# Performance work log

Hardware: AMD Instinct MI355X
Metric: run time of the kernel (lower is better)

## Reference

```python
import jax, jax.numpy as jnp
import numpy as np

NOISE_STD = 0.1
NUM_EXPERTS = 32
TOPK = 2
OUTPUT_DIM = 256


def setup_inputs() -> dict:
    key = jax.random.key(0)
    k_x, k_n, k_gw, k_ew = jax.random.split(key, 4)
    N, D_IN = 32768, 256
    E, D_OUT = NUM_EXPERTS, OUTPUT_DIM
    x = jax.random.normal(k_x, (N, D_IN), dtype=jnp.float32)
    noise = jax.random.normal(k_n, (N, E), dtype=jnp.float32)
    # gate: nn.Linear(input_dim, num_experts) default init scale
    gate_w = jax.random.normal(k_gw, (E, D_IN), dtype=jnp.float32) / jnp.sqrt(D_IN).astype(jnp.float32)
    gate_b = jnp.zeros((E,), dtype=jnp.float32)
    # experts: nn.Linear(input_dim, output_dim * num_experts), xavier_uniform weight, zero bias
    lim = float(np.sqrt(6.0 / (D_IN + D_OUT * E)))
    experts_w = jax.random.uniform(k_ew, (D_OUT * E, D_IN), minval=-lim, maxval=lim, dtype=jnp.float32)
    experts_b = jnp.zeros((D_OUT * E,), dtype=jnp.float32)
    return {"x": x, "noise": noise, "gate_w": gate_w, "gate_b": gate_b,
            "experts_w": experts_w, "experts_b": experts_b}


def reference(x, noise, gate_w, gate_b, experts_w, experts_b):
    N = x.shape[0]
    E, D = NUM_EXPERTS, OUTPUT_DIM
    # gating with noisy logits
    gate_logits = x @ gate_w.T + gate_b + noise * NOISE_STD          # [N, E]
    gate_probs = jax.nn.softmax(gate_logits, axis=-1)                # [N, E]
    # load-balance auxiliary loss
    gate_probs_mean = gate_probs.mean(axis=0)                        # [E]
    expected = 1.0 / E
    load_balance_loss = jnp.mean((gate_probs_mean - expected) ** 2) * E
    # top-k routing
    topk_probs, topk_idx = jax.lax.top_k(gate_probs, TOPK)           # [N, k]
    # all-expert dense linear, then gather the selected experts
    expert_outputs = (x @ experts_w.T + experts_b).reshape(N, E, D)  # [N, E, D]
    sel = jnp.take_along_axis(expert_outputs, topk_idx[:, :, None], axis=1)  # [N, k, D]
    output = jnp.einsum('bk,bkd->bd', topk_probs, sel)               # [N, D]
    return output, load_balance_loss
```

## Files before the change

kernel.cpp:

```cpp
#include <hip/hip_runtime.h>
#include <hip/hip_bf16.h>

#define N_ROWS 32768
#define D_INP  256
#define NEXP   32
#define D_OUTP 256
#define TROWS  64
#define NTILES 1056
#define GROWS  64

typedef __attribute__((ext_vector_type(4))) float f32x4;
typedef __attribute__((ext_vector_type(8))) short bf16x8;

__device__ inline unsigned short f2b(float f) {
    union { __hip_bfloat16 h; unsigned short u; } cv;
    cv.h = __float2bfloat16(f);
    return cv.u;
}
__device__ inline float b2f(unsigned short u) {
    union { unsigned v; float f; } c; c.v = ((unsigned)u) << 16; return c.f;
}

__global__ __launch_bounds__(256) void gate_kernel(
    const float* __restrict__ x, const float* __restrict__ noise,
    const float* __restrict__ gw, const float* __restrict__ gb,
    const float* __restrict__ ew, unsigned short* __restrict__ wbT,
    unsigned short* __restrict__ xb, float* __restrict__ tkp,
    int* __restrict__ tki, float* __restrict__ esum, int* __restrict__ ecnt)
{
    __shared__ float rA[8448];
    __shared__ float xs[64 * 68];
    __shared__ float lsum[NEXP];
    __shared__ int   lcnt[NEXP];

    int tid = threadIdx.x;
    int row0 = blockIdx.x * GROWS;

    #pragma unroll
    for (int it = 0; it < 8; ++it) {
        int q = it * 256 + tid;
        int e = q >> 6;
        int k = (q & 63) * 4;
        float4 v = ((const float4*)gw)[q];
        *(float4*)&rA[e * 260 + k] = v;
    }
    if (tid < NEXP) { lsum[tid] = 0.f; lcnt[tid] = 0; }

    int lane = tid & 63;
    int wid  = tid >> 6;
    int e4 = lane & 7;
    int rq = lane >> 3;

    float acc[8][4];
    #pragma unroll
    for (int m = 0; m < 8; m++)
        #pragma unroll
        for (int n = 0; n < 4; n++) acc[m][n] = 0.f;

    for (int s = 0; s < 4; ++s) {
        __syncthreads();
        #pragma unroll
        for (int it = 0; it < 4; ++it) {
            int q = it * 256 + tid;
            int r = q >> 4;
            int kq = q & 15;
            float4 v = *(const float4*)(x + (size_t)(row0 + r) * D_INP + s * 64 + kq * 4);
            *(float4*)&xs[r * 68 + kq * 4] = v;
            unsigned short b[4] = { f2b(v.x), f2b(v.y), f2b(v.z), f2b(v.w) };
            *(ushort4*)(xb + (size_t)(row0 + r) * D_INP + s * 64 + kq * 4) = *(ushort4*)b;
        }
        __syncthreads();
        int ko = s * 64 + wid * 16;
        #pragma unroll
        for (int c = 0; c < 4; ++c) {
            float4 wv[4];
            #pragma unroll
            for (int n = 0; n < 4; n++)
                wv[n] = *(float4*)&rA[(e4 + 8 * n) * 260 + ko + c * 4];
            #pragma unroll
            for (int m = 0; m < 8; m++) {
                float4 xv = *(float4*)&xs[(rq + 8 * m) * 68 + wid * 16 + c * 4];
                #pragma unroll
                for (int n = 0; n < 4; n++)
                    acc[m][n] = fmaf(xv.x, wv[n].x,
                                fmaf(xv.y, wv[n].y,
                                fmaf(xv.z, wv[n].z,
                                fmaf(xv.w, wv[n].w, acc[m][n]))));
            }
        }
    }
    __syncthreads();

    {
        int base = (wid * 64 + lane) * 33;
        #pragma unroll
        for (int m = 0; m < 8; m++)
            #pragma unroll
            for (int n = 0; n < 4; n++)
                rA[base + m * 4 + n] = acc[m][n];
    }
    __syncthreads();

    {
        int row = tid >> 2;
        int eo  = (tid & 3) * 8;
        int n   = tid & 3;
        int R = row0 + row;
        int j = (row >> 3) * 4 + n;
        int lpb = (row & 7) * 8;
        float4 nz0 = *(const float4*)(noise + (size_t)R * NEXP + eo);
        float4 nz1 = *(const float4*)(noise + (size_t)R * NEXP + eo + 4);
        float nz[8] = { nz0.x, nz0.y, nz0.z, nz0.w, nz1.x, nz1.y, nz1.z, nz1.w };
        float l[8], p[8];
        #pragma unroll
        for (int i = 0; i < 8; i++) {
            int a = (lpb + i) * 33 + j;
            float v = rA[a] + rA[2112 + a] + rA[4224 + a] + rA[6336 + a];
            l[i] = v + gb[eo + i] + 0.1f * nz[i];
        }
        float mx = l[0];
        #pragma unroll
        for (int i = 1; i < 8; i++) mx = fmaxf(mx, l[i]);
        mx = fmaxf(mx, __shfl_xor(mx, 1));
        mx = fmaxf(mx, __shfl_xor(mx, 2));
        float sum = 0.f;
        #pragma unroll
        for (int i = 0; i < 8; i++) { p[i] = expf(l[i] - mx); sum += p[i]; }
        sum += __shfl_xor(sum, 1);
        sum += __shfl_xor(sum, 2);
        float inv = 1.f / sum;
        #pragma unroll
        for (int i = 0; i < 8; i++) p[i] *= inv;

        float bp = p[0]; int bi = eo;
        #pragma unroll
        for (int i = 1; i < 8; i++) if (p[i] > bp) { bp = p[i]; bi = eo + i; }
        #pragma unroll
        for (int s2 = 1; s2 < 4; s2 <<= 1) {
            float op = __shfl_xor(bp, s2); int oi = __shfl_xor(bi, s2);
            if (op > bp || (op == bp && oi < bi)) { bp = op; bi = oi; }
        }
        float bp2 = -1.f; int bi2 = 0;
        #pragma unroll
        for (int i = 0; i < 8; i++) {
            int E = eo + i;
            float q = (E == bi) ? -1.f : p[i];
            if (q > bp2 || (q == bp2 && E < bi2)) { bp2 = q; bi2 = E; }
        }
        #pragma unroll
        for (int s2 = 1; s2 < 4; s2 <<= 1) {
            float op = __shfl_xor(bp2, s2); int oi = __shfl_xor(bi2, s2);
            if (op > bp2 || (op == bp2 && oi < bi2)) { bp2 = op; bi2 = oi; }
        }
        if ((tid & 3) == 0) {
            tkp[R * 2] = bp;  tkp[R * 2 + 1] = bp2;
            tki[R * 2] = bi;  tki[R * 2 + 1] = bi2;
            atomicAdd(&lcnt[bi], 1); atomicAdd(&lcnt[bi2], 1);
        }
        #pragma unroll
        for (int i = 0; i < 8; i++) atomicAdd(&lsum[eo + i], p[i]);
    }

    #pragma unroll
    for (int it = 0; it < 2; ++it) {
        int fid = blockIdx.x * 512 + it * 256 + tid;
        int row = fid >> 5;
        int kc  = fid & 31;
        const float4* sp = (const float4*)(ew + (size_t)row * D_INP + kc * 8);
        float4 v0 = sp[0], v1 = sp[1];
        unsigned short t[8] = { f2b(v0.x), f2b(v0.y), f2b(v0.z), f2b(v0.w),
                                f2b(v1.x), f2b(v1.y), f2b(v1.z), f2b(v1.w) };
        int e  = row >> 8;
        int rr = row & 255;
        int q  = rr >> 6;
        int nn = (rr >> 4) & 3;
        int lr = rr & 15;
        int kk = kc >> 2;
        int kg = kc & 3;
        size_t off = ((((size_t)(e * 4 + q) * 8 + kk) * 4 + nn) * 64 + kg * 16 + lr) * 8;
        *(uint4*)(wbT + off) = *(uint4*)t;
    }

    __syncthreads();
    if (tid < NEXP) {
        unsafeAtomicAdd(&esum[tid], lsum[tid]);
        atomicAdd(&ecnt[tid], lcnt[tid]);
    }
}

__global__ __launch_bounds__(1024) void build_list_kernel(
    const int* __restrict__ tki, const float* __restrict__ esum,
    const int* __restrict__ ecnt, int* __restrict__ cursor0,
    int* __restrict__ list, float* __restrict__ loss_out)
{
    __shared__ int lcnt[NEXP], lbase[NEXP], s_offs[NEXP + 1];
    int tid = threadIdx.x;
    if (tid < NEXP) lcnt[tid] = 0;
    if (tid < 32) {
        int c = ecnt[tid];
        int ic = c;
        #pragma unroll
        for (int s = 1; s < 32; s <<= 1) {
            int a = __shfl_up(ic, s, 32);
            if (tid >= s) ic += a;
        }
        s_offs[tid + 1] = ic;
        if (tid == 0) s_offs[0] = 0;
    }
    __syncthreads();
    int r = blockIdx.x * 1024 + tid;
    int e0 = tki[r * 2], e1 = tki[r * 2 + 1];
    int p0 = atomicAdd(&lcnt[e0], 1);
    int p1 = atomicAdd(&lcnt[e1], 1);
    __syncthreads();
    if (tid < NEXP) lbase[tid] = s_offs[tid] + atomicAdd(&cursor0[tid], lcnt[tid]);
    __syncthreads();
    list[lbase[e0] + p0] = r * 2;
    list[lbase[e1] + p1] = r * 2 + 1;

    if (blockIdx.x == 0 && tid < 32) {
        float d = esum[tid] * (1.f / N_ROWS) - (1.f / NEXP);
        float v = d * d;
        #pragma unroll
        for (int s = 16; s > 0; s >>= 1) v += __shfl_xor(v, s, 32);
        if (tid == 0) *loss_out = v;
    }
}

__global__ __launch_bounds__(256) void moe_gemm_kernel(
    const unsigned short* __restrict__ xb, const unsigned short* __restrict__ wbT,
    const float* __restrict__ expb, const float* __restrict__ tkp,
    const int* __restrict__ list, const int* __restrict__ ecnt,
    unsigned short* __restrict__ y0, unsigned short* __restrict__ y1)
{
    __shared__ int s_offs[NEXP + 1], s_toff[NEXP + 1];
    __shared__ unsigned short xa[TROWS * 256];
    __shared__ int   srow[TROWS];
    __shared__ int   sslot[TROWS];
    __shared__ float sprob[TROWS];

    int tid = threadIdx.x;
    if (tid < 32) {
        int c = ecnt[tid];
        int ic = c, itc = (c + TROWS - 1) >> 6;
        #pragma unroll
        for (int s = 1; s < 32; s <<= 1) {
            int a  = __shfl_up(ic, s, 32);  if (tid >= s) ic += a;
            int b2 = __shfl_up(itc, s, 32); if (tid >= s) itc += b2;
        }
        s_offs[tid + 1] = ic; s_toff[tid + 1] = itc;
        if (tid == 0) { s_offs[0] = 0; s_toff[0] = 0; }
    }
    __syncthreads();

    int b = (blockIdx.x & 7) * (NTILES / 8) + (blockIdx.x >> 3);
    if (b >= s_toff[NEXP]) return;
    int e = 0;
    #pragma unroll
    for (int s = 16; s; s >>= 1)
        if (e + s <= 31 && s_toff[e + s] <= b) e += s;
    int m0 = s_offs[e] + (b - s_toff[e]) * TROWS;
    int nr = min(TROWS, s_offs[e + 1] - m0);

    if (tid < TROWS) {
        if (tid < nr) {
            int ent = list[m0 + tid];
            srow[tid]  = ent >> 1;
            sslot[tid] = ent & 1;
            sprob[tid] = tkp[ent];
        } else { srow[tid] = -1; sslot[tid] = 0; sprob[tid] = 0.f; }
    }
    __syncthreads();

    {
        int r_ = tid >> 2;
        int gr = srow[r_]; if (gr < 0) gr = 0;
        const uint4* src = (const uint4*)(xb + (size_t)gr * D_INP);
        uint4* dst = (uint4*)xa;
        int swz = r_ & 7;
        #pragma unroll
        for (int i = 0; i < 8; ++i) {
            int c = (tid & 3) + 4 * i;
            dst[r_ * 32 + (c ^ swz)] = src[c];
        }
    }
    __syncthreads();

    int wave = tid >> 6;
    int lane = tid & 63;
    int lr = lane & 15;
    int kg = lane >> 4;
    int n0 = wave * 64;
    int aswz = lr & 7;

    const unsigned short* wbase = wbT + (size_t)(e * 4 + wave) * 32 * 512;

    f32x4 acc[4][4];
    #pragma unroll
    for (int mm = 0; mm < 4; mm++)
        #pragma unroll
        for (int nn = 0; nn < 4; nn++)
            acc[mm][nn] = (f32x4){0.f, 0.f, 0.f, 0.f};

    #pragma unroll
    for (int kk = 0; kk < 8; kk++) {
        int chunk = kk * 4 + kg;
        bf16x8 a[4], bb[4];
        #pragma unroll
        for (int mm = 0; mm < 4; mm++)
            a[mm] = *(const bf16x8*)&xa[(mm * 16 + lr) * 256 + ((chunk ^ aswz) * 8)];
        #pragma unroll
        for (int nn = 0; nn < 4; nn++)
            bb[nn] = *(const bf16x8*)(wbase + (kk * 4 + nn) * 512 + lane * 8);
        #pragma unroll
        for (int mm = 0; mm < 4; mm++)
            #pragma unroll
            for (int nn = 0; nn < 4; nn++)
                acc[mm][nn] = __builtin_amdgcn_mfma_f32_16x16x32_bf16(a[mm], bb[nn], acc[mm][nn], 0, 0, 0);
    }
    __syncthreads();

    {
        float bias[4];
        #pragma unroll
        for (int nn = 0; nn < 4; nn++) bias[nn] = expb[e * 256 + n0 + nn * 16 + lr];
        #pragma unroll
        for (int mm = 0; mm < 4; mm++) {
            #pragma unroll
            for (int j = 0; j < 4; j++) {
                int lrow = mm * 16 + kg * 4 + j;
                float pp = sprob[lrow];
                #pragma unroll
                for (int nn = 0; nn < 4; nn++) {
                    float v = (acc[mm][nn][j] + bias[nn]) * pp;
                    xa[lrow * 256 + n0 + nn * 16 + lr] = f2b(v);
                }
            }
        }
    }
    __syncthreads();

    {
        int r_ = tid >> 2;
        int gr = srow[r_];
        if (gr >= 0) {
            unsigned short* dstb = (sslot[r_] ? y1 : y0) + (size_t)gr * D_OUTP;
            const uint4* src = (const uint4*)(xa + r_ * 256);
            uint4* dst = (uint4*)dstb;
            #pragma unroll
            for (int i = 0; i < 8; ++i) {
                int c = (tid & 3) + 4 * i;
                dst[c] = src[c];
            }
        }
    }
}

__global__ __launch_bounds__(256) void combine_kernel(
    const unsigned short* __restrict__ y0, const unsigned short* __restrict__ y1,
    float* __restrict__ out)
{
    size_t i = ((size_t)blockIdx.x * 256 + threadIdx.x) * 8;
    uint4 a = *(const uint4*)(y0 + i);
    uint4 b = *(const uint4*)(y1 + i);
    const unsigned short* ap = (const unsigned short*)&a;
    const unsigned short* bp = (const unsigned short*)&b;
    float4 o0, o1;
    o0.x = b2f(ap[0]) + b2f(bp[0]);
    o0.y = b2f(ap[1]) + b2f(bp[1]);
    o0.z = b2f(ap[2]) + b2f(bp[2]);
    o0.w = b2f(ap[3]) + b2f(bp[3]);
    o1.x = b2f(ap[4]) + b2f(bp[4]);
    o1.y = b2f(ap[5]) + b2f(bp[5]);
    o1.z = b2f(ap[6]) + b2f(bp[6]);
    o1.w = b2f(ap[7]) + b2f(bp[7]);
    *(float4*)(out + i)     = o0;
    *(float4*)(out + i + 4) = o1;
}

extern "C" void kernel_launch(void* const* d_in, const int* in_sizes, int n_in,
                              void* d_out, int out_size, void* d_ws, size_t ws_size,
                              hipStream_t stream)
{
    const float* x   = (const float*)d_in[0];
    const float* noi = (const float*)d_in[1];
    const float* gw  = (const float*)d_in[2];
    const float* gb  = (const float*)d_in[3];
    const float* ew  = (const float*)d_in[4];
    const float* eb  = (const float*)d_in[5];
    float* out = (float*)d_out;

    char* p = (char*)d_ws;
    unsigned short* xb  = (unsigned short*)p; p += (size_t)N_ROWS * D_INP * 2;
    unsigned short* wbT = (unsigned short*)p; p += (size_t)NEXP * D_OUTP * D_INP * 2;
    unsigned short* y0  = (unsigned short*)p; p += (size_t)N_ROWS * D_OUTP * 2;
    unsigned short* y1  = (unsigned short*)p; p += (size_t)N_ROWS * D_OUTP * 2;
    float* tkp  = (float*)p; p += (size_t)N_ROWS * 2 * 4;
    int*   tki  = (int*)p;   p += (size_t)N_ROWS * 2 * 4;
    int*   list = (int*)p;   p += (size_t)N_ROWS * 2 * 4;
    float* esum = (float*)p; p += 32 * 4;
    int*   ecnt = (int*)p;   p += 32 * 4;
    int*   cur0 = (int*)p;   p += 32 * 4;

    hipMemsetAsync(esum, 0, 3 * 32 * 4, stream);

    gate_kernel<<<N_ROWS / GROWS, 256, 0, stream>>>(x, noi, gw, gb, ew, wbT, xb, tkp, tki, esum, ecnt);
    build_list_kernel<<<N_ROWS / 1024, 1024, 0, stream>>>(tki, esum, ecnt, cur0, list, out + (size_t)N_ROWS * D_OUTP);
    moe_gemm_kernel<<<NTILES, 256, 0, stream>>>(xb, wbT, eb, tkp, list, ecnt, y0, y1);
    combine_kernel<<<N_ROWS * D_OUTP / 8 / 256, 256, 0, stream>>>(y0, y1, out);
}
```

Before: 149.1 us.

## Make MoE GEMM persistent per expert with register-prefetched next tile

Replaces the flat grid of 1056 single-tile blocks with 512 blocks, 16 per expert, each looping over that expert's row tiles with a stride of 16. The gathered x rows for the next tile are loaded into registers while the current tile's MFMA runs, so the gather latency is meant to overlap with compute. Routing entries for two tiles are staged in shared memory at once. This depends on the 16 blocks per expert covering load imbalance. Experts with more tiles take proportionally longer, and the extra register buffer may reduce occupancy.

```diff
diff --git a/kernel.cpp b/kernel.cpp
--- a/kernel.cpp
+++ b/kernel.cpp
@@ -6,7 +6,7 @@
 #define NEXP   32
 #define D_OUTP 256
 #define TROWS  64
-#define NTILES 1056
+#define NBLK   512
 #define GROWS  64
 
 typedef __attribute__((ext_vector_type(4))) float f32x4;
@@ -233,125 +233,147 @@
     const int* __restrict__ list, const int* __restrict__ ecnt,
     unsigned short* __restrict__ y0, unsigned short* __restrict__ y1)
 {
-    __shared__ int s_offs[NEXP + 1], s_toff[NEXP + 1];
+    __shared__ int s_offs[NEXP + 1];
     __shared__ unsigned short xa[TROWS * 256];
-    __shared__ int   srow[TROWS];
-    __shared__ int   sslot[TROWS];
-    __shared__ float sprob[TROWS];
+    __shared__ int   entT[2][TROWS];
+    __shared__ float sprobT[2][TROWS];
 
     int tid = threadIdx.x;
     if (tid < 32) {
         int c = ecnt[tid];
-        int ic = c, itc = (c + TROWS - 1) >> 6;
+        int ic = c;
         #pragma unroll
         for (int s = 1; s < 32; s <<= 1) {
-            int a  = __shfl_up(ic, s, 32);  if (tid >= s) ic += a;
-            int b2 = __shfl_up(itc, s, 32); if (tid >= s) itc += b2;
-        }
-        s_offs[tid + 1] = ic; s_toff[tid + 1] = itc;
-        if (tid == 0) { s_offs[0] = 0; s_toff[0] = 0; }
-    }
-    __syncthreads();
-
-    int b = (blockIdx.x & 7) * (NTILES / 8) + (blockIdx.x >> 3);
-    if (b >= s_toff[NEXP]) return;
-    int e = 0;
-    #pragma unroll
-    for (int s = 16; s; s >>= 1)
-        if (e + s <= 31 && s_toff[e + s] <= b) e += s;
-    int m0 = s_offs[e] + (b - s_toff[e]) * TROWS;
-    int nr = min(TROWS, s_offs[e + 1] - m0);
-
-    if (tid < TROWS) {
-        if (tid < nr) {
-            int ent = list[m0 + tid];
-            srow[tid]  = ent >> 1;
-            sslot[tid] = ent & 1;
-            sprob[tid] = tkp[ent];
-        } else { srow[tid] = -1; sslot[tid] = 0; sprob[tid] = 0.f; }
-    }
-    __syncthreads();
-
-    {
-        int r_ = tid >> 2;
-        int gr = srow[r_]; if (gr < 0) gr = 0;
-        const uint4* src = (const uint4*)(xb + (size_t)gr * D_INP);
-        uint4* dst = (uint4*)xa;
-        int swz = r_ & 7;
-        #pragma unroll
-        for (int i = 0; i < 8; ++i) {
-            int c = (tid & 3) + 4 * i;
-            dst[r_ * 32 + (c ^ swz)] = src[c];
-        }
-    }
-    __syncthreads();
+            int a = __shfl_up(ic, s, 32);
+            if (tid >= s) ic += a;
+        }
+        s_offs[tid + 1] = ic;
+        if (tid == 0) s_offs[0] = 0;
+    }
+    __syncthreads();
+
+    int bs = (blockIdx.x & 7) * 64 + (blockIdx.x >> 3);
+    int e  = bs >> 4;
+    int j0 = bs & 15;
+    int base  = s_offs[e];
+    int cnt   = s_offs[e + 1] - base;
+    int ntile = (cnt + TROWS - 1) >> 6;
+    if (j0 >= ntile) return;
 
     int wave = tid >> 6;
     int lane = tid & 63;
     int lr = lane & 15;
     int kg = lane >> 4;
     int n0 = wave * 64;
+    int sr = tid >> 2;
+    int sc = tid & 3;
+    int swz = sr & 7;
     int aswz = lr & 7;
 
     const unsigned short* wbase = wbT + (size_t)(e * 4 + wave) * 32 * 512;
-
-    f32x4 acc[4][4];
+    float bias[4];
     #pragma unroll
-    for (int mm = 0; mm < 4; mm++)
-        #pragma unroll
-        for (int nn = 0; nn < 4; nn++)
-            acc[mm][nn] = (f32x4){0.f, 0.f, 0.f, 0.f};
-
-    #pragma unroll
-    for (int kk = 0; kk < 8; kk++) {
-        int chunk = kk * 4 + kg;
-        bf16x8 a[4], bb[4];
-        #pragma unroll
-        for (int mm = 0; mm < 4; mm++)
-            a[mm] = *(const bf16x8*)&xa[(mm * 16 + lr) * 256 + ((chunk ^ aswz) * 8)];
-        #pragma unroll
-        for (int nn = 0; nn < 4; nn++)
-            bb[nn] = *(const bf16x8*)(wbase + (kk * 4 + nn) * 512 + lane * 8);
-        #pragma unroll
-        for (int mm = 0; mm < 4; mm++)
-            #pragma unroll
-            for (int nn = 0; nn < 4; nn++)
-                acc[mm][nn] = __builtin_amdgcn_mfma_f32_16x16x32_bf16(a[mm], bb[nn], acc[mm][nn], 0, 0, 0);
-    }
-    __syncthreads();
-
-    {
-        float bias[4];
-        #pragma unroll
-        for (int nn = 0; nn < 4; nn++) bias[nn] = expb[e * 256 + n0 + nn * 16 + lr];
-        #pragma unroll
-        for (int mm = 0; mm < 4; mm++) {
-            #pragma unroll
-            for (int j = 0; j < 4; j++) {
-                int lrow = mm * 16 + kg * 4 + j;
-                float pp = sprob[lrow];
-                #pragma unroll
-                for (int nn = 0; nn < 4; nn++) {
-                    float v = (acc[mm][nn][j] + bias[nn]) * pp;
-                    xa[lrow * 256 + n0 + nn * 16 + lr] = f2b(v);
+    for (int nn = 0; nn < 4; nn++) bias[nn] = expb[e * 256 + n0 + nn * 16 + lr];
+
+    uint4 areg[8];
+
+    for (int t0 = j0; t0 < ntile; t0 += 32) {
+        if (tid < 128) {
+            int p = tid >> 6, r = tid & 63;
+            int tp = t0 + p * 16;
+            int ent = -1; float pr = 0.f;
+            if (tp < ntile && r < cnt - tp * TROWS) {
+                ent = list[base + tp * TROWS + r];
+                pr  = tkp[ent];
+            }
+            entT[p][r] = ent; sprobT[p][r] = pr;
+        }
+        __syncthreads();
+
+        {
+            int ent = entT[0][sr];
+            int gr = ent < 0 ? 0 : (ent >> 1);
+            const uint4* src = (const uint4*)(xb + (size_t)gr * D_INP);
+            #pragma unroll
+            for (int i = 0; i < 8; ++i) areg[i] = src[sc + 4 * i];
+        }
+
+        for (int p = 0; p < 2; ++p) {
+            int tp = t0 + p * 16;
+            if (tp >= ntile) break;
+
+            {
+                uint4* dst = (uint4*)xa;
+                #pragma unroll
+                for (int i = 0; i < 8; ++i) {
+                    int c = sc + 4 * i;
+                    dst[sr * 32 + (c ^ swz)] = areg[i];
                 }
             }
-        }
-    }
-    __syncthreads();
-
-    {
-        int r_ = tid >> 2;
-        int gr = srow[r_];
-        if (gr >= 0) {
-            unsigned short* dstb = (sslot[r_] ? y1 : y0) + (size_t)gr * D_OUTP;
-            const uint4* src = (const uint4*)(xa + r_ * 256);
-            uint4* dst = (uint4*)dstb;
-            #pragma unroll
-            for (int i = 0; i < 8; ++i) {
-                int c = (tid & 3) + 4 * i;
-                dst[c] = src[c];
-            }
+            __syncthreads();
+
+            if (p == 0 && t0 + 16 < ntile) {
+                int ent = entT[1][sr];
+                int gr = ent < 0 ? 0 : (ent >> 1);
+                const uint4* src = (const uint4*)(xb + (size_t)gr * D_INP);
+                #pragma unroll
+                for (int i = 0; i < 8; ++i) areg[i] = src[sc + 4 * i];
+            }
+
+            f32x4 acc[4][4];
+            #pragma unroll
+            for (int mm = 0; mm < 4; mm++)
+                #pragma unroll
+                for (int nn = 0; nn < 4; nn++)
+                    acc[mm][nn] = (f32x4){0.f, 0.f, 0.f, 0.f};
+
+            #pragma unroll
+            for (int kk = 0; kk < 8; kk++) {
+                int chunk = kk * 4 + kg;
+                bf16x8 a[4], bb[4];
+                #pragma unroll
+                for (int mm = 0; mm < 4; mm++)
+                    a[mm] = *(const bf16x8*)&xa[(mm * 16 + lr) * 256 + ((chunk ^ aswz) * 8)];
+                #pragma unroll
+                for (int nn = 0; nn < 4; nn++)
+                    bb[nn] = *(const bf16x8*)(wbase + (kk * 4 + nn) * 512 + lane * 8);
+                #pragma unroll
+                for (int mm = 0; mm < 4; mm++)
+                    #pragma unroll
+                    for (int nn = 0; nn < 4; nn++)
+                        acc[mm][nn] = __builtin_amdgcn_mfma_f32_16x16x32_bf16(a[mm], bb[nn], acc[mm][nn], 0, 0, 0);
+            }
+            __syncthreads();
+
+            #pragma unroll
+            for (int mm = 0; mm < 4; mm++) {
+                #pragma unroll
+                for (int j = 0; j < 4; j++) {
+                    int lrow = mm * 16 + kg * 4 + j;
+                    float pp = sprobT[p][lrow];
+                    #pragma unroll
+                    for (int nn = 0; nn < 4; nn++) {
+                        float v = (acc[mm][nn][j] + bias[nn]) * pp;
+                        xa[lrow * 256 + n0 + nn * 16 + lr] = f2b(v);
+                    }
+                }
+            }
+            __syncthreads();
+
+            {
+                int ent = entT[p][sr];
+                if (ent >= 0) {
+                    unsigned short* dstb = ((ent & 1) ? y1 : y0) + (size_t)(ent >> 1) * D_OUTP;
+                    const uint4* src = (const uint4*)(xa + sr * 256);
+                    uint4* dst = (uint4*)dstb;
+                    #pragma unroll
+                    for (int i = 0; i < 8; ++i) {
+                        int c = sc + 4 * i;
+                        dst[c] = src[c];
+                    }
+                }
+            }
+            __syncthreads();
         }
     }
 }
@@ -406,6 +428,6 @@
 
     gate_kernel<<<N_ROWS / GROWS, 256, 0, stream>>>(x, noi, gw, gb, ew, wbT, xb, tkp, tki, esum, ecnt);
     build_list_kernel<<<N_ROWS / 1024, 1024, 0, stream>>>(tki, esum, ecnt, cur0, list, out + (size_t)N_ROWS * D_OUTP);
-    moe_gemm_kernel<<<NTILES, 256, 0, stream>>>(xb, wbT, eb, tkp, list, ecnt, y0, y1);
+    moe_gemm_kernel<<<NBLK, 256, 0, stream>>>(xb, wbT, eb, tkp, list, ecnt, y0, y1);
     combine_kernel<<<N_ROWS * D_OUTP / 8 / 256, 256, 0, stream>>>(y0, y1, out);
 }
```

After: 168.2 us. +12.8%, slower.

## Fuse gating, list build, expert GEMM and combine into one persistent kernel

Applied to the files above, without the earlier changes.

Replaces the four separate launches with a single persistent kernel of 512 blocks that passes through each phase, separated by software grid barriers built on atomic counters. The GEMM phase now loops over 32-row tiles instead of 64-row tiles so the persistent blocks can balance the uneven expert tiles. This is meant to remove launch gaps and per-kernel tail effects between the small phases. In exchange it adds spin-wait barrier cost, relies on all 512 blocks being co-resident, and halves the MFMA work per weight fetch in the GEMM.

```diff
diff --git a/kernel.cpp b/kernel.cpp
--- a/kernel.cpp
+++ b/kernel.cpp
@@ -5,9 +5,9 @@
 #define D_INP  256
 #define NEXP   32
 #define D_OUTP 256
-#define TROWS  64
-#define NTILES 1056
+#define TROWS  32
 #define GROWS  64
+#define NBLKF  512
 
 typedef __attribute__((ext_vector_type(4))) float f32x4;
 typedef __attribute__((ext_vector_type(8))) short bf16x8;
@@ -21,361 +21,380 @@
     union { unsigned v; float f; } c; c.v = ((unsigned)u) << 16; return c.f;
 }
 
-__global__ __launch_bounds__(256) void gate_kernel(
+struct GateSh  { float rA[8448]; float xs[GROWS * 68]; float lsum[NEXP]; int lcnt[NEXP]; };
+struct GemmSh  { unsigned short xa[TROWS * 256]; int s_offs[NEXP + 1]; int s_toff[NEXP + 1];
+                 int srow[TROWS]; int sslot[TROWS]; float sprob[TROWS]; };
+struct BuildSh { int lcnt[NEXP]; int lbase[NEXP]; int soffs[NEXP + 1]; };
+union ShU { GateSh g; GemmSh m; BuildSh b; };
+
+__device__ __forceinline__ void gbar(int* cnt, int target) {
+    __threadfence();
+    __syncthreads();
+    if (threadIdx.x == 0) {
+        atomicAdd(cnt, 1);
+        while (atomicAdd(cnt, 0) < target) __builtin_amdgcn_s_sleep(2);
+    }
+    __syncthreads();
+    __threadfence();
+}
+
+__global__ __launch_bounds__(256, 2) void moe_fused(
     const float* __restrict__ x, const float* __restrict__ noise,
     const float* __restrict__ gw, const float* __restrict__ gb,
-    const float* __restrict__ ew, unsigned short* __restrict__ wbT,
-    unsigned short* __restrict__ xb, float* __restrict__ tkp,
-    int* __restrict__ tki, float* __restrict__ esum, int* __restrict__ ecnt)
-{
-    __shared__ float rA[8448];
-    __shared__ float xs[64 * 68];
-    __shared__ float lsum[NEXP];
-    __shared__ int   lcnt[NEXP];
-
-    int tid = threadIdx.x;
-    int row0 = blockIdx.x * GROWS;
-
-    #pragma unroll
-    for (int it = 0; it < 8; ++it) {
-        int q = it * 256 + tid;
-        int e = q >> 6;
-        int k = (q & 63) * 4;
-        float4 v = ((const float4*)gw)[q];
-        *(float4*)&rA[e * 260 + k] = v;
-    }
-    if (tid < NEXP) { lsum[tid] = 0.f; lcnt[tid] = 0; }
-
-    int lane = tid & 63;
-    int wid  = tid >> 6;
-    int e4 = lane & 7;
-    int rq = lane >> 3;
-
-    float acc[8][4];
-    #pragma unroll
-    for (int m = 0; m < 8; m++)
-        #pragma unroll
-        for (int n = 0; n < 4; n++) acc[m][n] = 0.f;
-
-    for (int s = 0; s < 4; ++s) {
-        __syncthreads();
-        #pragma unroll
-        for (int it = 0; it < 4; ++it) {
-            int q = it * 256 + tid;
-            int r = q >> 4;
-            int kq = q & 15;
-            float4 v = *(const float4*)(x + (size_t)(row0 + r) * D_INP + s * 64 + kq * 4);
-            *(float4*)&xs[r * 68 + kq * 4] = v;
-            unsigned short b[4] = { f2b(v.x), f2b(v.y), f2b(v.z), f2b(v.w) };
-            *(ushort4*)(xb + (size_t)(row0 + r) * D_INP + s * 64 + kq * 4) = *(ushort4*)b;
-        }
-        __syncthreads();
-        int ko = s * 64 + wid * 16;
-        #pragma unroll
-        for (int c = 0; c < 4; ++c) {
-            float4 wv[4];
-            #pragma unroll
-            for (int n = 0; n < 4; n++)
-                wv[n] = *(float4*)&rA[(e4 + 8 * n) * 260 + ko + c * 4];
-            #pragma unroll
-            for (int m = 0; m < 8; m++) {
-                float4 xv = *(float4*)&xs[(rq + 8 * m) * 68 + wid * 16 + c * 4];
-                #pragma unroll
-                for (int n = 0; n < 4; n++)
-                    acc[m][n] = fmaf(xv.x, wv[n].x,
-                                fmaf(xv.y, wv[n].y,
-                                fmaf(xv.z, wv[n].z,
-                                fmaf(xv.w, wv[n].w, acc[m][n]))));
-            }
-        }
-    }
-    __syncthreads();
-
-    {
-        int base = (wid * 64 + lane) * 33;
-        #pragma unroll
-        for (int m = 0; m < 8; m++)
-            #pragma unroll
-            for (int n = 0; n < 4; n++)
-                rA[base + m * 4 + n] = acc[m][n];
-    }
-    __syncthreads();
-
-    {
-        int row = tid >> 2;
-        int eo  = (tid & 3) * 8;
-        int n   = tid & 3;
-        int R = row0 + row;
-        int j = (row >> 3) * 4 + n;
-        int lpb = (row & 7) * 8;
-        float4 nz0 = *(const float4*)(noise + (size_t)R * NEXP + eo);
-        float4 nz1 = *(const float4*)(noise + (size_t)R * NEXP + eo + 4);
-        float nz[8] = { nz0.x, nz0.y, nz0.z, nz0.w, nz1.x, nz1.y, nz1.z, nz1.w };
-        float l[8], p[8];
-        #pragma unroll
-        for (int i = 0; i < 8; i++) {
-            int a = (lpb + i) * 33 + j;
-            float v = rA[a] + rA[2112 + a] + rA[4224 + a] + rA[6336 + a];
-            l[i] = v + gb[eo + i] + 0.1f * nz[i];
-        }
-        float mx = l[0];
-        #pragma unroll
-        for (int i = 1; i < 8; i++) mx = fmaxf(mx, l[i]);
-        mx = fmaxf(mx, __shfl_xor(mx, 1));
-        mx = fmaxf(mx, __shfl_xor(mx, 2));
-        float sum = 0.f;
-        #pragma unroll
-        for (int i = 0; i < 8; i++) { p[i] = expf(l[i] - mx); sum += p[i]; }
-        sum += __shfl_xor(sum, 1);
-        sum += __shfl_xor(sum, 2);
-        float inv = 1.f / sum;
-        #pragma unroll
-        for (int i = 0; i < 8; i++) p[i] *= inv;
-
-        float bp = p[0]; int bi = eo;
-        #pragma unroll
-        for (int i = 1; i < 8; i++) if (p[i] > bp) { bp = p[i]; bi = eo + i; }
-        #pragma unroll
-        for (int s2 = 1; s2 < 4; s2 <<= 1) {
-            float op = __shfl_xor(bp, s2); int oi = __shfl_xor(bi, s2);
-            if (op > bp || (op == bp && oi < bi)) { bp = op; bi = oi; }
-        }
-        float bp2 = -1.f; int bi2 = 0;
-        #pragma unroll
-        for (int i = 0; i < 8; i++) {
-            int E = eo + i;
-            float q = (E == bi) ? -1.f : p[i];
-            if (q > bp2 || (q == bp2 && E < bi2)) { bp2 = q; bi2 = E; }
-        }
-        #pragma unroll
-        for (int s2 = 1; s2 < 4; s2 <<= 1) {
-            float op = __shfl_xor(bp2, s2); int oi = __shfl_xor(bi2, s2);
-            if (op > bp2 || (op == bp2 && oi < bi2)) { bp2 = op; bi2 = oi; }
-        }
-        if ((tid & 3) == 0) {
-            tkp[R * 2] = bp;  tkp[R * 2 + 1] = bp2;
-            tki[R * 2] = bi;  tki[R * 2 + 1] = bi2;
-            atomicAdd(&lcnt[bi], 1); atomicAdd(&lcnt[bi2], 1);
-        }
-        #pragma unroll
-        for (int i = 0; i < 8; i++) atomicAdd(&lsum[eo + i], p[i]);
-    }
-
-    #pragma unroll
-    for (int it = 0; it < 2; ++it) {
-        int fid = blockIdx.x * 512 + it * 256 + tid;
-        int row = fid >> 5;
-        int kc  = fid & 31;
-        const float4* sp = (const float4*)(ew + (size_t)row * D_INP + kc * 8);
-        float4 v0 = sp[0], v1 = sp[1];
-        unsigned short t[8] = { f2b(v0.x), f2b(v0.y), f2b(v0.z), f2b(v0.w),
-                                f2b(v1.x), f2b(v1.y), f2b(v1.z), f2b(v1.w) };
-        int e  = row >> 8;
-        int rr = row & 255;
-        int q  = rr >> 6;
-        int nn = (rr >> 4) & 3;
-        int lr = rr & 15;
-        int kk = kc >> 2;
-        int kg = kc & 3;
-        size_t off = ((((size_t)(e * 4 + q) * 8 + kk) * 4 + nn) * 64 + kg * 16 + lr) * 8;
-        *(uint4*)(wbT + off) = *(uint4*)t;
-    }
-
-    __syncthreads();
-    if (tid < NEXP) {
-        unsafeAtomicAdd(&esum[tid], lsum[tid]);
-        atomicAdd(&ecnt[tid], lcnt[tid]);
-    }
-}
-
-__global__ __launch_bounds__(1024) void build_list_kernel(
-    const int* __restrict__ tki, const float* __restrict__ esum,
-    const int* __restrict__ ecnt, int* __restrict__ cursor0,
-    int* __restrict__ list, float* __restrict__ loss_out)
-{
-    __shared__ int lcnt[NEXP], lbase[NEXP], s_offs[NEXP + 1];
-    int tid = threadIdx.x;
-    if (tid < NEXP) lcnt[tid] = 0;
-    if (tid < 32) {
-        int c = ecnt[tid];
-        int ic = c;
-        #pragma unroll
-        for (int s = 1; s < 32; s <<= 1) {
-            int a = __shfl_up(ic, s, 32);
-            if (tid >= s) ic += a;
-        }
-        s_offs[tid + 1] = ic;
-        if (tid == 0) s_offs[0] = 0;
-    }
-    __syncthreads();
-    int r = blockIdx.x * 1024 + tid;
-    int e0 = tki[r * 2], e1 = tki[r * 2 + 1];
-    int p0 = atomicAdd(&lcnt[e0], 1);
-    int p1 = atomicAdd(&lcnt[e1], 1);
-    __syncthreads();
-    if (tid < NEXP) lbase[tid] = s_offs[tid] + atomicAdd(&cursor0[tid], lcnt[tid]);
-    __syncthreads();
-    list[lbase[e0] + p0] = r * 2;
-    list[lbase[e1] + p1] = r * 2 + 1;
-
-    if (blockIdx.x == 0 && tid < 32) {
-        float d = esum[tid] * (1.f / N_ROWS) - (1.f / NEXP);
-        float v = d * d;
-        #pragma unroll
-        for (int s = 16; s > 0; s >>= 1) v += __shfl_xor(v, s, 32);
-        if (tid == 0) *loss_out = v;
-    }
-}
-
-__global__ __launch_bounds__(256) void moe_gemm_kernel(
-    const unsigned short* __restrict__ xb, const unsigned short* __restrict__ wbT,
-    const float* __restrict__ expb, const float* __restrict__ tkp,
-    const int* __restrict__ list, const int* __restrict__ ecnt,
-    unsigned short* __restrict__ y0, unsigned short* __restrict__ y1)
-{
-    __shared__ int s_offs[NEXP + 1], s_toff[NEXP + 1];
-    __shared__ unsigned short xa[TROWS * 256];
-    __shared__ int   srow[TROWS];
-    __shared__ int   sslot[TROWS];
-    __shared__ float sprob[TROWS];
-
-    int tid = threadIdx.x;
-    if (tid < 32) {
-        int c = ecnt[tid];
-        int ic = c, itc = (c + TROWS - 1) >> 6;
-        #pragma unroll
-        for (int s = 1; s < 32; s <<= 1) {
-            int a  = __shfl_up(ic, s, 32);  if (tid >= s) ic += a;
-            int b2 = __shfl_up(itc, s, 32); if (tid >= s) itc += b2;
-        }
-        s_offs[tid + 1] = ic; s_toff[tid + 1] = itc;
-        if (tid == 0) { s_offs[0] = 0; s_toff[0] = 0; }
-    }
-    __syncthreads();
-
-    int b = (blockIdx.x & 7) * (NTILES / 8) + (blockIdx.x >> 3);
-    if (b >= s_toff[NEXP]) return;
-    int e = 0;
-    #pragma unroll
-    for (int s = 16; s; s >>= 1)
-        if (e + s <= 31 && s_toff[e + s] <= b) e += s;
-    int m0 = s_offs[e] + (b - s_toff[e]) * TROWS;
-    int nr = min(TROWS, s_offs[e + 1] - m0);
-
-    if (tid < TROWS) {
-        if (tid < nr) {
-            int ent = list[m0 + tid];
-            srow[tid]  = ent >> 1;
-            sslot[tid] = ent & 1;
-            sprob[tid] = tkp[ent];
-        } else { srow[tid] = -1; sslot[tid] = 0; sprob[tid] = 0.f; }
-    }
-    __syncthreads();
-
-    {
-        int r_ = tid >> 2;
-        int gr = srow[r_]; if (gr < 0) gr = 0;
-        const uint4* src = (const uint4*)(xb + (size_t)gr * D_INP);
-        uint4* dst = (uint4*)xa;
-        int swz = r_ & 7;
-        #pragma unroll
-        for (int i = 0; i < 8; ++i) {
-            int c = (tid & 3) + 4 * i;
-            dst[r_ * 32 + (c ^ swz)] = src[c];
-        }
-    }
-    __syncthreads();
-
-    int wave = tid >> 6;
-    int lane = tid & 63;
-    int lr = lane & 15;
-    int kg = lane >> 4;
-    int n0 = wave * 64;
-    int aswz = lr & 7;
-
-    const unsigned short* wbase = wbT + (size_t)(e * 4 + wave) * 32 * 512;
-
-    f32x4 acc[4][4];
-    #pragma unroll
-    for (int mm = 0; mm < 4; mm++)
-        #pragma unroll
-        for (int nn = 0; nn < 4; nn++)
-            acc[mm][nn] = (f32x4){0.f, 0.f, 0.f, 0.f};
-
-    #pragma unroll
-    for (int kk = 0; kk < 8; kk++) {
-        int chunk = kk * 4 + kg;
-        bf16x8 a[4], bb[4];
-        #pragma unroll
-        for (int mm = 0; mm < 4; mm++)
-            a[mm] = *(const bf16x8*)&xa[(mm * 16 + lr) * 256 + ((chunk ^ aswz) * 8)];
-        #pragma unroll
-        for (int nn = 0; nn < 4; nn++)
-            bb[nn] = *(const bf16x8*)(wbase + (kk * 4 + nn) * 512 + lane * 8);
-        #pragma unroll
-        for (int mm = 0; mm < 4; mm++)
-            #pragma unroll
-            for (int nn = 0; nn < 4; nn++)
-                acc[mm][nn] = __builtin_amdgcn_mfma_f32_16x16x32_bf16(a[mm], bb[nn], acc[mm][nn], 0, 0, 0);
-    }
-    __syncthreads();
-
-    {
-        float bias[4];
-        #pragma unroll
-        for (int nn = 0; nn < 4; nn++) bias[nn] = expb[e * 256 + n0 + nn * 16 + lr];
-        #pragma unroll
-        for (int mm = 0; mm < 4; mm++) {
-            #pragma unroll
-            for (int j = 0; j < 4; j++) {
-                int lrow = mm * 16 + kg * 4 + j;
-                float pp = sprob[lrow];
-                #pragma unroll
-                for (int nn = 0; nn < 4; nn++) {
-                    float v = (acc[mm][nn][j] + bias[nn]) * pp;
-                    xa[lrow * 256 + n0 + nn * 16 + lr] = f2b(v);
-                }
-            }
-        }
-    }
-    __syncthreads();
-
-    {
-        int r_ = tid >> 2;
-        int gr = srow[r_];
-        if (gr >= 0) {
-            unsigned short* dstb = (sslot[r_] ? y1 : y0) + (size_t)gr * D_OUTP;
-            const uint4* src = (const uint4*)(xa + r_ * 256);
-            uint4* dst = (uint4*)dstb;
-            #pragma unroll
-            for (int i = 0; i < 8; ++i) {
-                int c = (tid & 3) + 4 * i;
-                dst[c] = src[c];
-            }
-        }
-    }
-}
-
-__global__ __launch_bounds__(256) void combine_kernel(
-    const unsigned short* __restrict__ y0, const unsigned short* __restrict__ y1,
+    const float* __restrict__ ew, const float* __restrict__ expb,
+    unsigned short* __restrict__ wbT, unsigned short* __restrict__ xb,
+    float* __restrict__ tkp, int* __restrict__ tki,
+    float* __restrict__ esum, int* __restrict__ ecnt, int* __restrict__ cur0,
+    int* __restrict__ bar, int* __restrict__ list,
+    unsigned short* __restrict__ y0, unsigned short* __restrict__ y1,
     float* __restrict__ out)
 {
-    size_t i = ((size_t)blockIdx.x * 256 + threadIdx.x) * 8;
-    uint4 a = *(const uint4*)(y0 + i);
-    uint4 b = *(const uint4*)(y1 + i);
-    const unsigned short* ap = (const unsigned short*)&a;
-    const unsigned short* bp = (const unsigned short*)&b;
-    float4 o0, o1;
-    o0.x = b2f(ap[0]) + b2f(bp[0]);
-    o0.y = b2f(ap[1]) + b2f(bp[1]);
-    o0.z = b2f(ap[2]) + b2f(bp[2]);
-    o0.w = b2f(ap[3]) + b2f(bp[3]);
-    o1.x = b2f(ap[4]) + b2f(bp[4]);
-    o1.y = b2f(ap[5]) + b2f(bp[5]);
-    o1.z = b2f(ap[6]) + b2f(bp[6]);
-    o1.w = b2f(ap[7]) + b2f(bp[7]);
-    *(float4*)(out + i)     = o0;
-    *(float4*)(out + i + 4) = o1;
+    __shared__ ShU sh;
+    int tid = threadIdx.x;
+    int bid = blockIdx.x;
+
+    {
+        int row0 = bid * GROWS;
+
+        #pragma unroll
+        for (int it = 0; it < 8; ++it) {
+            int q = it * 256 + tid;
+            int e = q >> 6;
+            int k = (q & 63) * 4;
+            float4 v = ((const float4*)gw)[q];
+            *(float4*)&sh.g.rA[e * 260 + k] = v;
+        }
+        if (tid < NEXP) { sh.g.lsum[tid] = 0.f; sh.g.lcnt[tid] = 0; }
+
+        int lane = tid & 63;
+        int wid  = tid >> 6;
+        int e4 = lane & 7;
+        int rq = lane >> 3;
+
+        float acc[8][4];
+        #pragma unroll
+        for (int m = 0; m < 8; m++)
+            #pragma unroll
+            for (int n = 0; n < 4; n++) acc[m][n] = 0.f;
+
+        for (int s = 0; s < 4; ++s) {
+            __syncthreads();
+            #pragma unroll
+            for (int it = 0; it < 4; ++it) {
+                int q = it * 256 + tid;
+                int r = q >> 4;
+                int kq = q & 15;
+                float4 v = *(const float4*)(x + (size_t)(row0 + r) * D_INP + s * 64 + kq * 4);
+                *(float4*)&sh.g.xs[r * 68 + kq * 4] = v;
+                unsigned short b[4] = { f2b(v.x), f2b(v.y), f2b(v.z), f2b(v.w) };
+                *(ushort4*)(xb + (size_t)(row0 + r) * D_INP + s * 64 + kq * 4) = *(ushort4*)b;
+            }
+            __syncthreads();
+            int ko = s * 64 + wid * 16;
+            #pragma unroll
+            for (int c = 0; c < 4; ++c) {
+                float4 wv[4];
+                #pragma unroll
+                for (int n = 0; n < 4; n++)
+                    wv[n] = *(float4*)&sh.g.rA[(e4 + 8 * n) * 260 + ko + c * 4];
+                #pragma unroll
+                for (int m = 0; m < 8; m++) {
+                    float4 xv = *(float4*)&sh.g.xs[(rq + 8 * m) * 68 + wid * 16 + c * 4];
+                    #pragma unroll
+                    for (int n = 0; n < 4; n++)
+                        acc[m][n] = fmaf(xv.x, wv[n].x,
+                                    fmaf(xv.y, wv[n].y,
+                                    fmaf(xv.z, wv[n].z,
+                                    fmaf(xv.w, wv[n].w, acc[m][n]))));
+                }
+            }
+        }
+        __syncthreads();
+
+        {
+            int base = (wid * 64 + lane) * 33;
+            #pragma unroll
+            for (int m = 0; m < 8; m++)
+                #pragma unroll
+                for (int n = 0; n < 4; n++)
+                    sh.g.rA[base + m * 4 + n] = acc[m][n];
+        }
+        __syncthreads();
+
+        {
+            int row = tid >> 2;
+            int eo  = (tid & 3) * 8;
+            int n   = tid & 3;
+            int R = row0 + row;
+            int j = (row >> 3) * 4 + n;
+            int lpb = (row & 7) * 8;
+            float4 nz0 = *(const float4*)(noise + (size_t)R * NEXP + eo);
+            float4 nz1 = *(const float4*)(noise + (size_t)R * NEXP + eo + 4);
+            float nz[8] = { nz0.x, nz0.y, nz0.z, nz0.w, nz1.x, nz1.y, nz1.z, nz1.w };
+            float l[8], p[8];
+            #pragma unroll
+            for (int i = 0; i < 8; i++) {
+                int a = (lpb + i) * 33 + j;
+                float v = sh.g.rA[a] + sh.g.rA[2112 + a] + sh.g.rA[4224 + a] + sh.g.rA[6336 + a];
+                l[i] = v + gb[eo + i] + 0.1f * nz[i];
+            }
+            float mx = l[0];
+            #pragma unroll
+            for (int i = 1; i < 8; i++) mx = fmaxf(mx, l[i]);
+            mx = fmaxf(mx, __shfl_xor(mx, 1));
+            mx = fmaxf(mx, __shfl_xor(mx, 2));
+            float sum = 0.f;
+            #pragma unroll
+            for (int i = 0; i < 8; i++) { p[i] = expf(l[i] - mx); sum += p[i]; }
+            sum += __shfl_xor(sum, 1);
+            sum += __shfl_xor(sum, 2);
+            float inv = 1.f / sum;
+            #pragma unroll
+            for (int i = 0; i < 8; i++) p[i] *= inv;
+
+            float bp = p[0]; int bi = eo;
+            #pragma unroll
+            for (int i = 1; i < 8; i++) if (p[i] > bp) { bp = p[i]; bi = eo + i; }
+            #pragma unroll
+            for (int s2 = 1; s2 < 4; s2 <<= 1) {
+                float op = __shfl_xor(bp, s2); int oi = __shfl_xor(bi, s2);
+                if (op > bp || (op == bp && oi < bi)) { bp = op; bi = oi; }
+            }
+            float bp2 = -1.f; int bi2 = 0;
+            #pragma unroll
+            for (int i = 0; i < 8; i++) {
+                int E = eo + i;
+                float q = (E == bi) ? -1.f : p[i];
+                if (q > bp2 || (q == bp2 && E < bi2)) { bp2 = q; bi2 = E; }
+            }
+            #pragma unroll
+            for (int s2 = 1; s2 < 4; s2 <<= 1) {
+                float op = __shfl_xor(bp2, s2); int oi = __shfl_xor(bi2, s2);
+                if (op > bp2 || (op == bp2 && oi < bi2)) { bp2 = op; bi2 = oi; }
+            }
+            if ((tid & 3) == 0) {
+                tkp[R * 2] = bp;  tkp[R * 2 + 1] = bp2;
+                tki[R * 2] = bi;  tki[R * 2 + 1] = bi2;
+                atomicAdd(&sh.g.lcnt[bi], 1); atomicAdd(&sh.g.lcnt[bi2], 1);
+            }
+            #pragma unroll
+            for (int i = 0; i < 8; i++) atomicAdd(&sh.g.lsum[eo + i], p[i]);
+        }
+
+        #pragma unroll
+        for (int it = 0; it < 2; ++it) {
+            int fid = bid * 512 + it * 256 + tid;
+            int row = fid >> 5;
+            int kc  = fid & 31;
+            const float4* sp = (const float4*)(ew + (size_t)row * D_INP + kc * 8);
+            float4 v0 = sp[0], v1 = sp[1];
+            unsigned short t[8] = { f2b(v0.x), f2b(v0.y), f2b(v0.z), f2b(v0.w),
+                                    f2b(v1.x), f2b(v1.y), f2b(v1.z), f2b(v1.w) };
+            int e  = row >> 8;
+            int rr = row & 255;
+            int q  = rr >> 6;
+            int nn = (rr >> 4) & 3;
+            int lr = rr & 15;
+            int kk = kc >> 2;
+            int kg = kc & 3;
+            size_t off = ((((size_t)(e * 4 + q) * 8 + kk) * 4 + nn) * 64 + kg * 16 + lr) * 8;
+            *(uint4*)(wbT + off) = *(uint4*)t;
+        }
+
+        __syncthreads();
+        if (tid < NEXP) {
+            unsafeAtomicAdd(&esum[tid], sh.g.lsum[tid]);
+            atomicAdd(&ecnt[tid], sh.g.lcnt[tid]);
+        }
+    }
+
+    gbar(bar, NBLKF);
+
+    if (bid < 32) {
+        if (tid < NEXP) sh.b.lcnt[tid] = 0;
+        if (tid < 32) {
+            int c = ecnt[tid];
+            int ic = c;
+            #pragma unroll
+            for (int s = 1; s < 32; s <<= 1) {
+                int a = __shfl_up(ic, s, 32);
+                if (tid >= s) ic += a;
+            }
+            sh.b.soffs[tid + 1] = ic;
+            if (tid == 0) sh.b.soffs[0] = 0;
+        }
+        __syncthreads();
+        int e0a[4], e1a[4], p0a[4], p1a[4];
+        #pragma unroll
+        for (int i = 0; i < 4; i++) {
+            int r = bid * 1024 + i * 256 + tid;
+            e0a[i] = tki[r * 2]; e1a[i] = tki[r * 2 + 1];
+            p0a[i] = atomicAdd(&sh.b.lcnt[e0a[i]], 1);
+            p1a[i] = atomicAdd(&sh.b.lcnt[e1a[i]], 1);
+        }
+        __syncthreads();
+        if (tid < NEXP) sh.b.lbase[tid] = sh.b.soffs[tid] + atomicAdd(&cur0[tid], sh.b.lcnt[tid]);
+        __syncthreads();
+        #pragma unroll
+        for (int i = 0; i < 4; i++) {
+            int r = bid * 1024 + i * 256 + tid;
+            list[sh.b.lbase[e0a[i]] + p0a[i]] = r * 2;
+            list[sh.b.lbase[e1a[i]] + p1a[i]] = r * 2 + 1;
+        }
+        if (bid == 0 && tid < 32) {
+            float d = esum[tid] * (1.f / N_ROWS) - (1.f / NEXP);
+            float v = d * d;
+            #pragma unroll
+            for (int s = 16; s > 0; s >>= 1) v += __shfl_xor(v, s, 32);
+            if (tid == 0) out[(size_t)N_ROWS * D_OUTP] = v;
+        }
+    }
+
+    gbar(bar, 2 * NBLKF);
+
+    {
+        if (tid < 32) {
+            int c = ecnt[tid];
+            int ic = c, itc = (c + TROWS - 1) >> 5;
+            #pragma unroll
+            for (int s = 1; s < 32; s <<= 1) {
+                int a  = __shfl_up(ic, s, 32);  if (tid >= s) ic += a;
+                int b2 = __shfl_up(itc, s, 32); if (tid >= s) itc += b2;
+            }
+            sh.m.s_offs[tid + 1] = ic; sh.m.s_toff[tid + 1] = itc;
+            if (tid == 0) { sh.m.s_offs[0] = 0; sh.m.s_toff[0] = 0; }
+        }
+        __syncthreads();
+        int ntile = sh.m.s_toff[NEXP];
+        int bs = (bid & 7) * 64 + (bid >> 3);
+
+        int wave = tid >> 6;
+        int lane = tid & 63;
+        int lr = lane & 15;
+        int kg = lane >> 4;
+        int n0 = wave * 64;
+        int aswz = lr & 7;
+        int sr = tid >> 3;
+        int sc = tid & 7;
+        int swz = sr & 7;
+
+        for (int t = bs; t < ntile; t += NBLKF) {
+            int e = 0;
+            #pragma unroll
+            for (int s = 16; s; s >>= 1)
+                if (e + s <= 31 && sh.m.s_toff[e + s] <= t) e += s;
+            int m0 = sh.m.s_offs[e] + (t - sh.m.s_toff[e]) * TROWS;
+            int nr = min(TROWS, sh.m.s_offs[e + 1] - m0);
+
+            __syncthreads();
+            if (tid < TROWS) {
+                if (tid < nr) {
+                    int ent = list[m0 + tid];
+                    sh.m.srow[tid]  = ent >> 1;
+                    sh.m.sslot[tid] = ent & 1;
+                    sh.m.sprob[tid] = tkp[ent];
+                } else { sh.m.srow[tid] = -1; sh.m.sslot[tid] = 0; sh.m.sprob[tid] = 0.f; }
+            }
+            __syncthreads();
+
+            {
+                int gr = sh.m.srow[sr]; if (gr < 0) gr = 0;
+                const uint4* src = (const uint4*)(xb + (size_t)gr * D_INP);
+                uint4* dst = (uint4*)sh.m.xa;
+                #pragma unroll
+                for (int i = 0; i < 4; ++i) {
+                    int c = sc + 8 * i;
+                    dst[sr * 32 + (c ^ swz)] = src[c];
+                }
+            }
+            __syncthreads();
+
+            const unsigned short* wbase = wbT + (size_t)(e * 4 + wave) * 32 * 512;
+            f32x4 acc[2][4];
+            #pragma unroll
+            for (int mm = 0; mm < 2; mm++)
+                #pragma unroll
+                for (int nn = 0; nn < 4; nn++)
+                    acc[mm][nn] = (f32x4){0.f, 0.f, 0.f, 0.f};
+
+            #pragma unroll
+            for (int kk = 0; kk < 8; kk++) {
+                int chunk = kk * 4 + kg;
+                bf16x8 a[2], bb[4];
+                #pragma unroll
+                for (int mm = 0; mm < 2; mm++)
+                    a[mm] = *(const bf16x8*)&sh.m.xa[(mm * 16 + lr) * 256 + ((chunk ^ aswz) * 8)];
+                #pragma unroll
+                for (int nn = 0; nn < 4; nn++)
+                    bb[nn] = *(const bf16x8*)(wbase + (kk * 4 + nn) * 512 + lane * 8);
+                #pragma unroll
+                for (int mm = 0; mm < 2; mm++)
+                    #pragma unroll
+                    for (int nn = 0; nn < 4; nn++)
+                        acc[mm][nn] = __builtin_amdgcn_mfma_f32_16x16x32_bf16(a[mm], bb[nn], acc[mm][nn], 0, 0, 0);
+            }
+            __syncthreads();
+
+            {
+                float bias[4];
+                #pragma unroll
+                for (int nn = 0; nn < 4; nn++) bias[nn] = expb[e * 256 + n0 + nn * 16 + lr];
+                #pragma unroll
+                for (int mm = 0; mm < 2; mm++) {
+                    #pragma unroll
+                    for (int j = 0; j < 4; j++) {
+                        int lrow = mm * 16 + kg * 4 + j;
+                        float pp = sh.m.sprob[lrow];
+                        #pragma unroll
+                        for (int nn = 0; nn < 4; nn++) {
+                            float v = (acc[mm][nn][j] + bias[nn]) * pp;
+                            sh.m.xa[lrow * 256 + n0 + nn * 16 + lr] = f2b(v);
+                        }
+                    }
+                }
+            }
+            __syncthreads();
+
+            {
+                int gr = sh.m.srow[sr];
+                if (gr >= 0) {
+                    unsigned short* dstb = (sh.m.sslot[sr] ? y1 : y0) + (size_t)gr * D_OUTP;
+                    const uint4* src = (const uint4*)(sh.m.xa + sr * 256);
+                    uint4* dst = (uint4*)dstb;
+                    #pragma unroll
+                    for (int i = 0; i < 4; ++i) {
+                        int c = sc + 8 * i;
+                        dst[c] = src[c];
+                    }
+                }
+            }
+        }
+    }
+
+    gbar(bar, 3 * NBLKF);
+
+    {
+        #pragma unroll
+        for (int i = 0; i < 8; ++i) {
+            size_t u = ((size_t)bid * 8 + i) * 256 + tid;
+            size_t off = u * 8;
+            uint4 a = *(const uint4*)(y0 + off);
+            uint4 b = *(const uint4*)(y1 + off);
+            const unsigned short* ap = (const unsigned short*)&a;
+            const unsigned short* bp = (const unsigned short*)&b;
+            float4 o0, o1;
+            o0.x = b2f(ap[0]) + b2f(bp[0]);
+            o0.y = b2f(ap[1]) + b2f(bp[1]);
+            o0.z = b2f(ap[2]) + b2f(bp[2]);
+            o0.w = b2f(ap[3]) + b2f(bp[3]);
+            o1.x = b2f(ap[4]) + b2f(bp[4]);
+            o1.y = b2f(ap[5]) + b2f(bp[5]);
+            o1.z = b2f(ap[6]) + b2f(bp[6]);
+            o1.w = b2f(ap[7]) + b2f(bp[7]);
+            *(float4*)(out + off)     = o0;
+            *(float4*)(out + off + 4) = o1;
+        }
+    }
 }
 
 extern "C" void kernel_launch(void* const* d_in, const int* in_sizes, int n_in,
@@ -401,11 +420,11 @@
     float* esum = (float*)p; p += 32 * 4;
     int*   ecnt = (int*)p;   p += 32 * 4;
     int*   cur0 = (int*)p;   p += 32 * 4;
-
-    hipMemsetAsync(esum, 0, 3 * 32 * 4, stream);
-
-    gate_kernel<<<N_ROWS / GROWS, 256, 0, stream>>>(x, noi, gw, gb, ew, wbT, xb, tkp, tki, esum, ecnt);
-    build_list_kernel<<<N_ROWS / 1024, 1024, 0, stream>>>(tki, esum, ecnt, cur0, list, out + (size_t)N_ROWS * D_OUTP);
-    moe_gemm_kernel<<<NTILES, 256, 0, stream>>>(xb, wbT, eb, tkp, list, ecnt, y0, y1);
-    combine_kernel<<<N_ROWS * D_OUTP / 8 / 256, 256, 0, stream>>>(y0, y1, out);
+    int*   bar  = (int*)p;   p += 4 * 4;
+
+    hipMemsetAsync(esum, 0, (3 * 32 + 4) * 4, stream);
+
+    moe_fused<<<NBLKF, 256, 0, stream>>>(x, noi, gw, gb, ew, eb, wbT, xb,
+                                         tkp, tki, esum, ecnt, cur0, bar, list,
+                                         y0, y1, out);
 }
```

Measured after the change: 463.1 us. 211% more time.
